# Kernel optimization log

Measured on AMD Instinct MI355X. Metric: run time of the kernel, lower is better.

## Reference

```python
import jax, jax.numpy as jnp
import numpy as np

H2 = 512    # internal hidden = hidden_size*2
E = 128     # embedding_size
V = 50000   # vocabulary_size
L = 512     # max_length (encoder input length)
B = 128     # batch


def setup_inputs() -> dict:
    key = jax.random.key(0)
    ks = jax.random.split(key, 20)
    s = 0.02
    return {
        "input_ids": jax.random.randint(ks[0], (B,), 0, V),
        "hidden": jax.random.normal(ks[1], (1, B, H2), jnp.float32),
        "encoder_outputs": jax.random.normal(ks[2], (L, B, H2), jnp.float32),
        "full_input": jax.random.randint(ks[3], (L, B), 0, V),
        # parameters
        "embedding": jax.random.normal(ks[4], (V, E), jnp.float32) * s,
        "W_ih": jax.random.normal(ks[5], (3 * H2, E), jnp.float32) * s,
        "W_hh": jax.random.normal(ks[6], (3 * H2, H2), jnp.float32) * s,
        "b_ih": jnp.zeros((3 * H2,), jnp.float32),
        "b_hh": jnp.zeros((3 * H2,), jnp.float32),
        "W_ds": jax.random.normal(ks[7], (H2, H2), jnp.float32) * s,
        "b_ds": jnp.zeros((H2,), jnp.float32),
        "w_h": jax.random.normal(ks[8], (H2,), jnp.float32),
        "att_v": jax.random.normal(ks[9], (H2,), jnp.float32),
        "W_oh": jax.random.normal(ks[10], (E, 2 * H2), jnp.float32) * s,
        "b_oh": jnp.zeros((E,), jnp.float32),
        "W_ov": jax.random.normal(ks[11], (V, E), jnp.float32) * s,
        "b_ov": jnp.zeros((V,), jnp.float32),
        "W_ptr": jax.random.normal(ks[12], (1, 2 * H2 + E), jnp.float32) * s,
        "b_ptr": jnp.zeros((1,), jnp.float32),
    }


def reference(input_ids, hidden, encoder_outputs, full_input, embedding,
              W_ih, W_hh, b_ih, b_hh, W_ds, b_ds, w_h, att_v,
              W_oh, b_oh, W_ov, b_ov, W_ptr, b_ptr):
    Bn = input_ids.shape[0]
    Ln = encoder_outputs.shape[0]
    Vn = embedding.shape[0]

    emb = embedding[input_ids]                       # [B, E] (dropout = identity in eval)
    h0 = hidden[0]                                   # [B, 2h]

    # single GRU step (PyTorch gate order r, z, n)
    gx = emb @ W_ih.T + b_ih                         # [B, 3*2h]
    gh = h0 @ W_hh.T + b_hh
    xr, xz, xn = jnp.split(gx, 3, axis=1)
    hr, hz, hn = jnp.split(gh, 3, axis=1)
    r = jax.nn.sigmoid(xr + hr)
    z = jax.nn.sigmoid(xz + hz)
    n = jnp.tanh(xn + r * hn)
    h_new = (1.0 - z) * n + z * h0                   # [B, 2h]

    # Bahdanau-style attention (faithful to source, incl. softmax over dim=1 = batch axis)
    dsl = h_new @ W_ds.T + b_ds                      # [B, 2h]
    att = jnp.tanh(w_h * encoder_outputs + dsl[None])  # [L, B, 2h]
    scores = (att_v * att).sum(-1)                   # [L, B]
    attn = jax.nn.softmax(scores, axis=1)            # torch F.softmax(dim=1)

    context = jnp.einsum('lb,lbh->bh', attn, encoder_outputs)  # [B, 2h]
    combined = jnp.concatenate([h_new, context], axis=1)        # [B, 4h]

    p_vocab = jax.nn.softmax((combined @ W_oh.T + b_oh) @ W_ov.T + b_ov, axis=1)  # [B, V]

    p_gen = jax.nn.sigmoid(jnp.concatenate([combined, emb], axis=1) @ W_ptr.T + b_ptr)  # [B, 1]

    # scatter attention mass onto extended vocab (copy distribution)
    token_input_dist = jnp.zeros((Bn, Vn + Ln), p_vocab.dtype).at[
        jnp.arange(Bn)[:, None], full_input.T
    ].add(attn.T)

    pad = jnp.zeros((Bn, Ln), p_vocab.dtype)
    p_final = jnp.concatenate([p_vocab * p_gen, pad], axis=1) + (1.0 - p_gen) * token_input_dist
    return (p_final, h_new[None], attn)
```

## Files before the change

kernel.cpp:

```cpp
#include <hip/hip_runtime.h>
#include <math.h>

#define B_  128
#define E_  128
#define H2_ 512
#define H3_ 1536
#define L_  512
#define V_  50000
#define VL_ 50512

typedef short bf16x8 __attribute__((ext_vector_type(8)));
typedef float f32x4 __attribute__((ext_vector_type(4)));

__device__ __forceinline__ float fast_tanh(float x) {
    float e = __expf(2.f * x);
    return 1.f - 2.f / (e + 1.f);
}
__device__ __forceinline__ float fast_sigmoid(float x) {
    return 1.f / (1.f + __expf(-x));
}
__device__ __forceinline__ short f2bf(float f) {
    unsigned u = __float_as_uint(f);
    u += 0x7fff + ((u >> 16) & 1);
    return (short)(u >> 16);
}

__global__ void k_gates(const int* __restrict__ ids, const float* __restrict__ tab,
                        const float* __restrict__ hidden,
                        const float* __restrict__ W_ih, const float* __restrict__ W_hh,
                        float* __restrict__ gxp, float* __restrict__ ghp) {
    __shared__ float As[32][36];
    __shared__ float Ws[32][36];
    int z = blockIdx.z;
    int which = (z < 2) ? 0 : 1;
    int kbeg  = which ? (z - 2) * 128 : z * 64;
    int kiter = which ? 4 : 2;
    const float* W = which ? W_hh : W_ih;
    int ldw = which ? H2_ : E_;
    float* C = which ? (ghp + (size_t)(z - 2) * B_ * H3_) : (gxp + (size_t)z * B_ * H3_);
    int bm = blockIdx.x * 32, bn = blockIdx.y * 32;
    int tid = threadIdx.x;
    int tm0 = (tid / 16) * 2, tn0 = (tid % 16) * 2;
    float acc[2][2] = {};
    for (int it = 0; it < kiter; ++it) {
        int k0 = kbeg + it * 32;
        for (int v = tid; v < 256; v += 256) {
            int m = v >> 3, q = (v & 7) << 2;
            int gm = bm + m;
            const float* arow = which ? (hidden + (size_t)gm * H2_)
                                      : (tab + (size_t)ids[gm] * E_);
            float4 x = *(const float4*)(arow + k0 + q);
            As[q+0][m] = x.x; As[q+1][m] = x.y; As[q+2][m] = x.z; As[q+3][m] = x.w;
        }
        for (int v = tid; v < 256; v += 256) {
            int n = v >> 3, q = (v & 7) << 2;
            float4 x = *(const float4*)(W + (size_t)(bn + n) * ldw + k0 + q);
            Ws[q+0][n] = x.x; Ws[q+1][n] = x.y; Ws[q+2][n] = x.z; Ws[q+3][n] = x.w;
        }
        __syncthreads();
        #pragma unroll
        for (int kk = 0; kk < 32; ++kk) {
            float a0 = As[kk][tm0], a1 = As[kk][tm0+1];
            float w0 = Ws[kk][tn0], w1 = Ws[kk][tn0+1];
            acc[0][0] += a0*w0; acc[0][1] += a0*w1;
            acc[1][0] += a1*w0; acc[1][1] += a1*w1;
        }
        __syncthreads();
    }
    #pragma unroll
    for (int i = 0; i < 2; ++i)
        #pragma unroll
        for (int j = 0; j < 2; ++j)
            C[(size_t)(bm+tm0+i) * H3_ + bn+tn0+j] = acc[i][j];
}

template<int BM, int BN, int BK, int TM, int TN, int SPLITK, bool ATOMIC>
__global__ void gemm_t(const float* __restrict__ A, int lda,
                       const float* __restrict__ W, int ldw,
                       float* __restrict__ C, int ldc,
                       int N, int K, int partElems) {
    __shared__ float As[BK][BM + 4];
    __shared__ float Ws[BK][BN + 4];
    int bm = blockIdx.x * BM, bn = blockIdx.y * BN;
    int tid = threadIdx.x;
    constexpr int NT = BN / TN;
    int tm0 = (tid / NT) * TM;
    int tn0 = (tid % NT) * TN;
    int kchunk = K / SPLITK;
    int kbeg = blockIdx.z * kchunk;
    float acc[TM][TN] = {};
    for (int k0 = kbeg; k0 < kbeg + kchunk; k0 += BK) {
        #pragma unroll
        for (int v = tid; v < BM * BK / 4; v += 256) {
            int m = v / (BK / 4), q = (v % (BK / 4)) * 4;
            float4 x = *(const float4*)(A + (size_t)(bm + m) * lda + k0 + q);
            As[q+0][m] = x.x; As[q+1][m] = x.y; As[q+2][m] = x.z; As[q+3][m] = x.w;
        }
        #pragma unroll
        for (int v = tid; v < BN * BK / 4; v += 256) {
            int n = v / (BK / 4), q = (v % (BK / 4)) * 4;
            float4 x = *(const float4*)(W + (size_t)(bn + n) * ldw + k0 + q);
            Ws[q+0][n] = x.x; Ws[q+1][n] = x.y; Ws[q+2][n] = x.z; Ws[q+3][n] = x.w;
        }
        __syncthreads();
        #pragma unroll
        for (int kk = 0; kk < BK; ++kk) {
            float a[TM], w[TN];
            #pragma unroll
            for (int i = 0; i < TM; ++i) a[i] = As[kk][tm0 + i];
            #pragma unroll
            for (int j = 0; j < TN; ++j) w[j] = Ws[kk][tn0 + j];
            #pragma unroll
            for (int i = 0; i < TM; ++i)
                #pragma unroll
                for (int j = 0; j < TN; ++j) acc[i][j] += a[i] * w[j];
        }
        __syncthreads();
    }
    float* Cz = ATOMIC ? C : (C + (size_t)blockIdx.z * partElems);
    #pragma unroll
    for (int i = 0; i < TM; ++i)
        #pragma unroll
        for (int j = 0; j < TN; ++j) {
            if (ATOMIC) atomicAdd(&Cz[(size_t)(bm+tm0+i) * ldc + bn+tn0+j], acc[i][j]);
            else        Cz[(size_t)(bm+tm0+i) * ldc + bn+tn0+j] = acc[i][j];
        }
}

__global__ void k_gru(const float* __restrict__ gxp, const float* __restrict__ ghp,
                      const float* __restrict__ b_ih, const float* __restrict__ b_hh,
                      const float* __restrict__ h0, const float* __restrict__ b_oh,
                      float* __restrict__ comb, float* __restrict__ hout,
                      float* __restrict__ hid, float* __restrict__ rsum8) {
    int idx = blockIdx.x * blockDim.x + threadIdx.x;
    int b = idx >> 9, h = idx & 511;
    const float* gx0 = gxp + (size_t)b * H3_;
    const float* gx1 = gx0 + (size_t)B_ * H3_;
    float xr = gx0[h]         + gx1[h]         + b_ih[h];
    float xz = gx0[H2_+h]     + gx1[H2_+h]     + b_ih[H2_+h];
    float xn = gx0[2*H2_+h]   + gx1[2*H2_+h]   + b_ih[2*H2_+h];
    float hr = b_hh[h], hz = b_hh[H2_+h], hn = b_hh[2*H2_+h];
    #pragma unroll
    for (int z = 0; z < 4; ++z) {
        const float* g = ghp + ((size_t)z * B_ + b) * H3_;
        hr += g[h]; hz += g[H2_+h]; hn += g[2*H2_+h];
    }
    float r = fast_sigmoid(xr + hr);
    float zz = fast_sigmoid(xz + hz);
    float n = fast_tanh(xn + r * hn);
    float hv = (1.f - zz) * n + zz * h0[idx];
    comb[b * (2 * H2_) + h] = hv;
    hout[idx] = hv;
    if (idx < B_ * E_) hid[idx] = b_oh[idx & 127];
    if (idx < 1024)    rsum8[idx] = 0.f;
}

__global__ void k_scores(const float* __restrict__ enc, const float* __restrict__ dslp,
                         const float* __restrict__ b_ds,
                         const float* __restrict__ w_h, const float* __restrict__ att_v,
                         float* __restrict__ scores) {
    int wid = (blockIdx.x << 2) + (threadIdx.x >> 6);
    int lane = threadIdx.x & 63;
    int b = wid & 127, lg = wid >> 7;
    int l0 = lg << 3;
    const float4* w4 = (const float4*)w_h;
    const float4* v4 = (const float4*)att_v;
    const float4* bd4 = (const float4*)b_ds;
    float4 d0 = bd4[lane], d1 = bd4[lane + 64];
    #pragma unroll
    for (int z = 0; z < 4; ++z) {
        const float4* dp = (const float4*)(dslp + (size_t)z * B_ * H2_ + b * H2_);
        float4 p0 = dp[lane], p1 = dp[lane + 64];
        d0.x += p0.x; d0.y += p0.y; d0.z += p0.z; d0.w += p0.w;
        d1.x += p1.x; d1.y += p1.y; d1.z += p1.z; d1.w += p1.w;
    }
    float4 w0 = w4[lane], w1 = w4[lane + 64];
    float4 v0 = v4[lane], v1 = v4[lane + 64];
    float4 e0[8], e1[8];
    #pragma unroll
    for (int q = 0; q < 8; ++q) {
        const float4* e4 = (const float4*)(enc + ((size_t)((l0 + q) * B_ + b)) * H2_);
        e0[q] = e4[lane];
        e1[q] = e4[lane + 64];
    }
    float s[8];
    #pragma unroll
    for (int q = 0; q < 8; ++q) {
        float t;
        t  = v0.x * fast_tanh(w0.x * e0[q].x + d0.x);
        t += v0.y * fast_tanh(w0.y * e0[q].y + d0.y);
        t += v0.z * fast_tanh(w0.z * e0[q].z + d0.z);
        t += v0.w * fast_tanh(w0.w * e0[q].w + d0.w);
        t += v1.x * fast_tanh(w1.x * e1[q].x + d1.x);
        t += v1.y * fast_tanh(w1.y * e1[q].y + d1.y);
        t += v1.z * fast_tanh(w1.z * e1[q].z + d1.z);
        t += v1.w * fast_tanh(w1.w * e1[q].w + d1.w);
        s[q] = t;
    }
    #pragma unroll
    for (int q = 0; q < 8; ++q) {
        float t = s[q];
        #pragma unroll
        for (int o = 32; o; o >>= 1) t += __shfl_xor(t, o);
        if (lane == 0) scores[(l0 + q) * B_ + b] = t;
    }
}

__global__ void k_softmax(const float* __restrict__ scores, float* __restrict__ attn) {
    int l = blockIdx.x, lane = threadIdx.x;
    float s0 = scores[l * B_ + lane], s1 = scores[l * B_ + lane + 64];
    float m = fmaxf(s0, s1);
    #pragma unroll
    for (int o = 32; o; o >>= 1) m = fmaxf(m, __shfl_xor(m, o));
    float e0 = __expf(s0 - m), e1 = __expf(s1 - m);
    float t = e0 + e1;
    #pragma unroll
    for (int o = 32; o; o >>= 1) t += __shfl_xor(t, o);
    float inv = 1.f / t;
    attn[l * B_ + lane] = e0 * inv;
    attn[l * B_ + lane + 64] = e1 * inv;
}

__global__ void k_context(const float* __restrict__ enc, const float* __restrict__ attn,
                          float* __restrict__ ctxp) {
    int b = blockIdx.x;
    int l0 = blockIdx.y << 6;
    int tid = threadIdx.x;
    __shared__ float a_s[64];
    if (tid < 64) a_s[tid] = attn[(l0 + tid) * B_ + b];
    __syncthreads();
    const float4* e = (const float4*)(enc + ((size_t)l0 * B_ + b) * H2_) + tid;
    float4 c = make_float4(0.f, 0.f, 0.f, 0.f);
    #pragma unroll 8
    for (int i = 0; i < 64; ++i) {
        float4 x = e[(size_t)i * (B_ * H2_ / 4)];
        float a = a_s[i];
        c.x += a * x.x; c.y += a * x.y; c.z += a * x.z; c.w += a * x.w;
    }
    ((float4*)(ctxp + ((size_t)blockIdx.y * B_ + b) * H2_))[tid] = c;
}

__global__ void k_ctxpgen(const float* __restrict__ ctxp, const int* __restrict__ ids,
                          const float* __restrict__ tab, const float* __restrict__ W_ptr,
                          const float* __restrict__ b_ptr,
                          float* __restrict__ comb, float* __restrict__ pgen) {
    __shared__ float red[128];
    int b = blockIdx.x, tid = threadIdx.x;
    float4 c = make_float4(0.f, 0.f, 0.f, 0.f);
    #pragma unroll
    for (int z = 0; z < 8; ++z) {
        float4 x = ((const float4*)(ctxp + ((size_t)z * B_ + b) * H2_))[tid];
        c.x += x.x; c.y += x.y; c.z += x.z; c.w += x.w;
    }
    ((float4*)(comb + b * (2 * H2_) + H2_))[tid] = c;
    const float4* wp = (const float4*)W_ptr;
    float4 wc = wp[128 + tid];
    float s = c.x * wc.x + c.y * wc.y + c.z * wc.z + c.w * wc.w;
    float4 hv = ((const float4*)(comb + b * (2 * H2_)))[tid];
    float4 wh = wp[tid];
    s += hv.x * wh.x + hv.y * wh.y + hv.z * wh.z + hv.w * wh.w;
    if (tid < 32) {
        float4 ev = ((const float4*)(tab + (size_t)ids[b] * E_))[tid];
        float4 we = wp[256 + tid];
        s += ev.x * we.x + ev.y * we.y + ev.z * we.z + ev.w * we.w;
    }
    red[tid] = s;
    __syncthreads();
    if (tid < 64) {
        float t = red[tid] + red[tid + 64];
        #pragma unroll
        for (int o = 32; o; o >>= 1) t += __shfl_xor(t, o);
        if (tid == 0) pgen[b] = fast_sigmoid(t + b_ptr[0]);
    }
}

__global__ void k_vsum(const float* __restrict__ hid, const float* __restrict__ Wov,
                       const float* __restrict__ bov, float* __restrict__ rsum8) {
    __shared__ float sm[4][128];
    int L = threadIdx.x & 63, w = threadIdx.x >> 6;
    int lrow = L & 15, lk = L >> 4;
    int n0 = blockIdx.x * 128 + w * 32;

    bf16x8 bfr[2][4];
    #pragma unroll
    for (int nt = 0; nt < 2; ++nt) {
        int n = n0 + nt * 16 + lrow;
        #pragma unroll
        for (int kk = 0; kk < 4; ++kk) {
            bf16x8 f;
            if (n < V_) {
                const float* p = Wov + (size_t)n * 128 + kk * 32 + lk * 8;
                float4 x = *(const float4*)p, y = *(const float4*)(p + 4);
                f[0]=f2bf(x.x); f[1]=f2bf(x.y); f[2]=f2bf(x.z); f[3]=f2bf(x.w);
                f[4]=f2bf(y.x); f[5]=f2bf(y.y); f[6]=f2bf(y.z); f[7]=f2bf(y.w);
            } else {
                #pragma unroll
                for (int j = 0; j < 8; ++j) f[j] = 0;
            }
            bfr[nt][kk] = f;
        }
    }
    f32x4 acc[8][2] = {};
    #pragma unroll
    for (int mt = 0; mt < 8; ++mt) {
        bf16x8 afr[4];
        #pragma unroll
        for (int kk = 0; kk < 4; ++kk) {
            const float* p = hid + (size_t)(mt * 16 + lrow) * 128 + kk * 32 + lk * 8;
            float4 x = *(const float4*)p, y = *(const float4*)(p + 4);
            bf16x8 f;
            f[0]=f2bf(x.x); f[1]=f2bf(x.y); f[2]=f2bf(x.z); f[3]=f2bf(x.w);
            f[4]=f2bf(y.x); f[5]=f2bf(y.y); f[6]=f2bf(y.z); f[7]=f2bf(y.w);
            afr[kk] = f;
        }
        #pragma unroll
        for (int nt = 0; nt < 2; ++nt)
            #pragma unroll
            for (int kk = 0; kk < 4; ++kk)
                acc[mt][nt] = __builtin_amdgcn_mfma_f32_16x16x32_bf16(
                    afr[kk], bfr[nt][kk], acc[mt][nt], 0, 0, 0);
    }
    float bv[2];
    #pragma unroll
    for (int nt = 0; nt < 2; ++nt) {
        int n = n0 + nt * 16 + lrow;
        bv[nt] = (n < V_) ? bov[n] : 0.f;
    }
    float rs[8][4];
    #pragma unroll
    for (int mt = 0; mt < 8; ++mt) {
        #pragma unroll
        for (int r = 0; r < 4; ++r) rs[mt][r] = 0.f;
        #pragma unroll
        for (int nt = 0; nt < 2; ++nt) {
            int n = n0 + nt * 16 + lrow;
            if (n < V_) {
                #pragma unroll
                for (int r = 0; r < 4; ++r)
                    rs[mt][r] += __expf(acc[mt][nt][r] + bv[nt]);
            }
        }
    }
    #pragma unroll
    for (int o = 1; o < 16; o <<= 1)
        #pragma unroll
        for (int mt = 0; mt < 8; ++mt)
            #pragma unroll
            for (int r = 0; r < 4; ++r) rs[mt][r] += __shfl_xor(rs[mt][r], o);
    if (lrow == 0) {
        #pragma unroll
        for (int mt = 0; mt < 8; ++mt)
            #pragma unroll
            for (int r = 0; r < 4; ++r)
                sm[w][mt * 16 + lk * 4 + r] = rs[mt][r];
    }
    __syncthreads();
    if (threadIdx.x < 128) {
        float p = sm[0][threadIdx.x] + sm[1][threadIdx.x]
                + sm[2][threadIdx.x] + sm[3][threadIdx.x];
        atomicAdd(&rsum8[(blockIdx.x & 7) * 128 + threadIdx.x], p);
    }
}

__global__ void k_vwrite(const float* __restrict__ hid, const float* __restrict__ Wov,
                         const float* __restrict__ bov, const float* __restrict__ pgen,
                         const float* __restrict__ rsum8, float* __restrict__ out) {
    __shared__ float scs[128];
    if (blockIdx.x == 391) {
        for (int i = threadIdx.x; i < B_ * (L_ / 4); i += 256) {
            int b = i >> 7, k = i & 127;
            ((float4*)(out + (size_t)b * VL_ + V_))[k] = make_float4(0.f,0.f,0.f,0.f);
        }
        return;
    }
    if (threadIdx.x < 128) {
        float s = 0.f;
        #pragma unroll
        for (int j = 0; j < 8; ++j) s += rsum8[j * 128 + threadIdx.x];
        scs[threadIdx.x] = pgen[threadIdx.x] / s;
    }
    __syncthreads();
    int L = threadIdx.x & 63, w = threadIdx.x >> 6;
    int lrow = L & 15, lk = L >> 4;
    int n0 = blockIdx.x * 128 + w * 32;

    bf16x8 bfr[2][4];
    #pragma unroll
    for (int nt = 0; nt < 2; ++nt) {
        int n = n0 + nt * 16 + lrow;
        #pragma unroll
        for (int kk = 0; kk < 4; ++kk) {
            bf16x8 f;
            if (n < V_) {
                const float* p = Wov + (size_t)n * 128 + kk * 32 + lk * 8;
                float4 x = *(const float4*)p, y = *(const float4*)(p + 4);
                f[0]=f2bf(x.x); f[1]=f2bf(x.y); f[2]=f2bf(x.z); f[3]=f2bf(x.w);
                f[4]=f2bf(y.x); f[5]=f2bf(y.y); f[6]=f2bf(y.z); f[7]=f2bf(y.w);
            } else {
                #pragma unroll
                for (int j = 0; j < 8; ++j) f[j] = 0;
            }
            bfr[nt][kk] = f;
        }
    }
    f32x4 acc[8][2] = {};
    #pragma unroll
    for (int mt = 0; mt < 8; ++mt) {
        bf16x8 afr[4];
        #pragma unroll
        for (int kk = 0; kk < 4; ++kk) {
            const float* p = hid + (size_t)(mt * 16 + lrow) * 128 + kk * 32 + lk * 8;
            float4 x = *(const float4*)p, y = *(const float4*)(p + 4);
            bf16x8 f;
            f[0]=f2bf(x.x); f[1]=f2bf(x.y); f[2]=f2bf(x.z); f[3]=f2bf(x.w);
            f[4]=f2bf(y.x); f[5]=f2bf(y.y); f[6]=f2bf(y.z); f[7]=f2bf(y.w);
            afr[kk] = f;
        }
        #pragma unroll
        for (int nt = 0; nt < 2; ++nt)
            #pragma unroll
            for (int kk = 0; kk < 4; ++kk)
                acc[mt][nt] = __builtin_amdgcn_mfma_f32_16x16x32_bf16(
                    afr[kk], bfr[nt][kk], acc[mt][nt], 0, 0, 0);
    }
    float bv[2];
    #pragma unroll
    for (int nt = 0; nt < 2; ++nt) {
        int n = n0 + nt * 16 + lrow;
        bv[nt] = (n < V_) ? bov[n] : 0.f;
    }
    #pragma unroll
    for (int mt = 0; mt < 8; ++mt) {
        #pragma unroll
        for (int nt = 0; nt < 2; ++nt) {
            int n = n0 + nt * 16 + lrow;
            if (n < V_) {
                #pragma unroll
                for (int r = 0; r < 4; ++r) {
                    int row = mt * 16 + lk * 4 + r;
                    out[(size_t)row * VL_ + n] =
                        __expf(acc[mt][nt][r] + bv[nt]) * scs[row];
                }
            }
        }
    }
}

__global__ void k_scatter(float* __restrict__ out, const int* __restrict__ full_input,
                          const float* __restrict__ attn, const float* __restrict__ pgen) {
    int idx = blockIdx.x * blockDim.x + threadIdx.x;
    int b = idx & 127;
    int tok = full_input[idx];
    atomicAdd(&out[(size_t)b * VL_ + tok], (1.f - pgen[b]) * attn[idx]);
}

extern "C" void kernel_launch(void* const* d_in, const int* in_sizes, int n_in,
                              void* d_out, int out_size, void* d_ws, size_t ws_size,
                              hipStream_t stream) {
    const int*   input_ids = (const int*)d_in[0];
    const float* hidden    = (const float*)d_in[1];
    const float* enc       = (const float*)d_in[2];
    const int*   full_in   = (const int*)d_in[3];
    const float* emb_tab   = (const float*)d_in[4];
    const float* W_ih      = (const float*)d_in[5];
    const float* W_hh      = (const float*)d_in[6];
    const float* b_ih      = (const float*)d_in[7];
    const float* b_hh      = (const float*)d_in[8];
    const float* W_ds      = (const float*)d_in[9];
    const float* b_ds      = (const float*)d_in[10];
    const float* w_h       = (const float*)d_in[11];
    const float* att_v     = (const float*)d_in[12];
    const float* W_oh      = (const float*)d_in[13];
    const float* b_oh      = (const float*)d_in[14];
    const float* W_ov      = (const float*)d_in[15];
    const float* b_ov      = (const float*)d_in[16];
    const float* W_ptr     = (const float*)d_in[17];
    const float* b_ptr     = (const float*)d_in[18];

    float* out = (float*)d_out;
    float* p_final = out;
    float* h_out   = out + (size_t)B_ * VL_;
    float* attn    = out + (size_t)B_ * VL_ + B_ * H2_;

    float* ws = (float*)d_ws;
    float* gxp    = ws;
    float* ghp    = gxp + 393216;
    float* comb   = ghp + 786432;
    float* dslp   = comb + 131072;
    float* scores = dslp + 262144;
    float* ctxp   = scores + 65536;
    float* hid    = ctxp + 524288;
    float* pgen   = hid + 16384;
    float* rsum8  = pgen + 128;

    k_gates<<<dim3(4,48,6), dim3(256), 0, stream>>>(input_ids, emb_tab, hidden,
                                                    W_ih, W_hh, gxp, ghp);
    k_gru<<<dim3(256), dim3(256), 0, stream>>>(gxp, ghp, b_ih, b_hh, hidden, b_oh,
                                               comb, h_out, hid, rsum8);
    gemm_t<32,32,32,2,2,4,false><<<dim3(4,16,4), dim3(256), 0, stream>>>(
        comb, 2*H2_, W_ds, H2_, dslp, H2_, H2_, H2_, B_*H2_);
    k_scores<<<dim3(2048), dim3(256), 0, stream>>>(enc, dslp, b_ds, w_h, att_v, scores);
    k_softmax<<<dim3(L_), dim3(64), 0, stream>>>(scores, attn);
    k_context<<<dim3(B_, 8), dim3(128), 0, stream>>>(enc, attn, ctxp);
    k_ctxpgen<<<dim3(B_), dim3(128), 0, stream>>>(ctxp, input_ids, emb_tab,
                                                  W_ptr, b_ptr, comb, pgen);
    gemm_t<32,32,32,2,2,8,true><<<dim3(4,4,8), dim3(256), 0, stream>>>(
        comb, 2*H2_, W_oh, 2*H2_, hid, E_, E_, 2*H2_, 0);
    k_vsum<<<dim3(391), dim3(256), 0, stream>>>(hid, W_ov, b_ov, rsum8);
    k_vwrite<<<dim3(392), dim3(256), 0, stream>>>(hid, W_ov, b_ov, pgen, rsum8, p_final);
    k_scatter<<<dim3(L_*B_/256), dim3(256), 0, stream>>>(p_final, full_in, attn, pgen);
}
```

Before: 140.6 us.

## Fuse attention scores, softmax and context into one kernel; fold W_oh into pgen

Merges the score, softmax and context kernels into a single k_attn kernel. Each block handles 4 encoder positions across the whole batch, so the batch-axis softmax can be done in shared memory and the encoder tile is re-read while still in cache. The W_ds GEMM now accumulates atomically into a bias-initialised buffer instead of writing split-K partials, and the W_oh projection moves into the context/pgen kernel. This removes several launches and the intermediate score and partial buffers. In exchange, the context reduction now sums 128 partials per batch row instead of 8, and the W_oh matvec runs serially per thread.

```diff
diff --git a/kernel.cpp b/kernel.cpp
--- a/kernel.cpp
+++ b/kernel.cpp
@@ -74,11 +74,10 @@
             C[(size_t)(bm+tm0+i) * H3_ + bn+tn0+j] = acc[i][j];
 }
 
-template<int BM, int BN, int BK, int TM, int TN, int SPLITK, bool ATOMIC>
-__global__ void gemm_t(const float* __restrict__ A, int lda,
-                       const float* __restrict__ W, int ldw,
-                       float* __restrict__ C, int ldc,
-                       int N, int K, int partElems) {
+template<int BM, int BN, int BK, int TM, int TN, int SPLITK>
+__global__ void gemm_atomic(const float* __restrict__ A, int lda,
+                            const float* __restrict__ W, int ldw,
+                            float* __restrict__ C, int ldc, int N, int K) {
     __shared__ float As[BK][BM + 4];
     __shared__ float Ws[BK][BN + 4];
     int bm = blockIdx.x * BM, bn = blockIdx.y * BN;
@@ -117,21 +116,18 @@
         }
         __syncthreads();
     }
-    float* Cz = ATOMIC ? C : (C + (size_t)blockIdx.z * partElems);
     #pragma unroll
     for (int i = 0; i < TM; ++i)
         #pragma unroll
-        for (int j = 0; j < TN; ++j) {
-            if (ATOMIC) atomicAdd(&Cz[(size_t)(bm+tm0+i) * ldc + bn+tn0+j], acc[i][j]);
-            else        Cz[(size_t)(bm+tm0+i) * ldc + bn+tn0+j] = acc[i][j];
-        }
+        for (int j = 0; j < TN; ++j)
+            atomicAdd(&C[(size_t)(bm+tm0+i) * ldc + bn+tn0+j], acc[i][j]);
 }
 
 __global__ void k_gru(const float* __restrict__ gxp, const float* __restrict__ ghp,
                       const float* __restrict__ b_ih, const float* __restrict__ b_hh,
-                      const float* __restrict__ h0, const float* __restrict__ b_oh,
+                      const float* __restrict__ h0, const float* __restrict__ b_ds,
                       float* __restrict__ comb, float* __restrict__ hout,
-                      float* __restrict__ hid, float* __restrict__ rsum8) {
+                      float* __restrict__ dsl, float* __restrict__ rsum8) {
     int idx = blockIdx.x * blockDim.x + threadIdx.x;
     int b = idx >> 9, h = idx & 511;
     const float* gx0 = gxp + (size_t)b * H3_;
@@ -151,127 +147,122 @@
     float hv = (1.f - zz) * n + zz * h0[idx];
     comb[b * (2 * H2_) + h] = hv;
     hout[idx] = hv;
-    if (idx < B_ * E_) hid[idx] = b_oh[idx & 127];
-    if (idx < 1024)    rsum8[idx] = 0.f;
-}
-
-__global__ void k_scores(const float* __restrict__ enc, const float* __restrict__ dslp,
-                         const float* __restrict__ b_ds,
-                         const float* __restrict__ w_h, const float* __restrict__ att_v,
-                         float* __restrict__ scores) {
-    int wid = (blockIdx.x << 2) + (threadIdx.x >> 6);
-    int lane = threadIdx.x & 63;
-    int b = wid & 127, lg = wid >> 7;
-    int l0 = lg << 3;
-    const float4* w4 = (const float4*)w_h;
-    const float4* v4 = (const float4*)att_v;
-    const float4* bd4 = (const float4*)b_ds;
-    float4 d0 = bd4[lane], d1 = bd4[lane + 64];
-    #pragma unroll
-    for (int z = 0; z < 4; ++z) {
-        const float4* dp = (const float4*)(dslp + (size_t)z * B_ * H2_ + b * H2_);
-        float4 p0 = dp[lane], p1 = dp[lane + 64];
-        d0.x += p0.x; d0.y += p0.y; d0.z += p0.z; d0.w += p0.w;
-        d1.x += p1.x; d1.y += p1.y; d1.z += p1.z; d1.w += p1.w;
-    }
-    float4 w0 = w4[lane], w1 = w4[lane + 64];
-    float4 v0 = v4[lane], v1 = v4[lane + 64];
-    float4 e0[8], e1[8];
-    #pragma unroll
-    for (int q = 0; q < 8; ++q) {
-        const float4* e4 = (const float4*)(enc + ((size_t)((l0 + q) * B_ + b)) * H2_);
-        e0[q] = e4[lane];
-        e1[q] = e4[lane + 64];
-    }
-    float s[8];
-    #pragma unroll
-    for (int q = 0; q < 8; ++q) {
-        float t;
-        t  = v0.x * fast_tanh(w0.x * e0[q].x + d0.x);
-        t += v0.y * fast_tanh(w0.y * e0[q].y + d0.y);
-        t += v0.z * fast_tanh(w0.z * e0[q].z + d0.z);
-        t += v0.w * fast_tanh(w0.w * e0[q].w + d0.w);
-        t += v1.x * fast_tanh(w1.x * e1[q].x + d1.x);
-        t += v1.y * fast_tanh(w1.y * e1[q].y + d1.y);
-        t += v1.z * fast_tanh(w1.z * e1[q].z + d1.z);
-        t += v1.w * fast_tanh(w1.w * e1[q].w + d1.w);
-        s[q] = t;
-    }
-    #pragma unroll
-    for (int q = 0; q < 8; ++q) {
-        float t = s[q];
-        #pragma unroll
-        for (int o = 32; o; o >>= 1) t += __shfl_xor(t, o);
-        if (lane == 0) scores[(l0 + q) * B_ + b] = t;
-    }
-}
-
-__global__ void k_softmax(const float* __restrict__ scores, float* __restrict__ attn) {
-    int l = blockIdx.x, lane = threadIdx.x;
-    float s0 = scores[l * B_ + lane], s1 = scores[l * B_ + lane + 64];
-    float m = fmaxf(s0, s1);
-    #pragma unroll
-    for (int o = 32; o; o >>= 1) m = fmaxf(m, __shfl_xor(m, o));
-    float e0 = __expf(s0 - m), e1 = __expf(s1 - m);
-    float t = e0 + e1;
-    #pragma unroll
-    for (int o = 32; o; o >>= 1) t += __shfl_xor(t, o);
-    float inv = 1.f / t;
-    attn[l * B_ + lane] = e0 * inv;
-    attn[l * B_ + lane + 64] = e1 * inv;
-}
-
-__global__ void k_context(const float* __restrict__ enc, const float* __restrict__ attn,
-                          float* __restrict__ ctxp) {
-    int b = blockIdx.x;
-    int l0 = blockIdx.y << 6;
-    int tid = threadIdx.x;
-    __shared__ float a_s[64];
-    if (tid < 64) a_s[tid] = attn[(l0 + tid) * B_ + b];
-    __syncthreads();
-    const float4* e = (const float4*)(enc + ((size_t)l0 * B_ + b) * H2_) + tid;
-    float4 c = make_float4(0.f, 0.f, 0.f, 0.f);
-    #pragma unroll 8
-    for (int i = 0; i < 64; ++i) {
-        float4 x = e[(size_t)i * (B_ * H2_ / 4)];
-        float a = a_s[i];
-        c.x += a * x.x; c.y += a * x.y; c.z += a * x.z; c.w += a * x.w;
-    }
-    ((float4*)(ctxp + ((size_t)blockIdx.y * B_ + b) * H2_))[tid] = c;
-}
-
-__global__ void k_ctxpgen(const float* __restrict__ ctxp, const int* __restrict__ ids,
-                          const float* __restrict__ tab, const float* __restrict__ W_ptr,
-                          const float* __restrict__ b_ptr,
-                          float* __restrict__ comb, float* __restrict__ pgen) {
+    dsl[idx] = b_ds[h];
+    if (idx < 1024) rsum8[idx] = 0.f;
+}
+
+__global__ __launch_bounds__(1024, 4)
+void k_attn(const float* __restrict__ enc, const float* __restrict__ dsl,
+            const float* __restrict__ w_h, const float* __restrict__ att_v,
+            float* __restrict__ attn, float* __restrict__ pctx) {
+    __shared__ float sp[8][16][2];
+    __shared__ float attn_lds[128];
+    int t = threadIdx.x;
+    int g = t >> 7;
+    int h4 = t & 127;
+    int lane = t & 63;
+    int w2 = (t >> 6) & 1;
+    float4 wv = ((const float4*)w_h)[h4];
+    float4 vv = ((const float4*)att_v)[h4];
+    float4 acc[16];
+    #pragma unroll
+    for (int i = 0; i < 16; ++i) acc[i] = make_float4(0.f, 0.f, 0.f, 0.f);
+    int l0 = blockIdx.x << 2;
+    for (int lj = 0; lj < 4; ++lj) {
+        int l = l0 + lj;
+        #pragma unroll
+        for (int i = 0; i < 16; ++i) {
+            int b = g + (i << 3);
+            float4 e = ((const float4*)enc)[((size_t)l * B_ + b) * 128 + h4];
+            float4 d = ((const float4*)dsl)[b * 128 + h4];
+            float p;
+            p  = vv.x * fast_tanh(wv.x * e.x + d.x);
+            p += vv.y * fast_tanh(wv.y * e.y + d.y);
+            p += vv.z * fast_tanh(wv.z * e.z + d.z);
+            p += vv.w * fast_tanh(wv.w * e.w + d.w);
+            #pragma unroll
+            for (int o = 32; o; o >>= 1) p += __shfl_xor(p, o);
+            if (lane == 0) sp[g][i][w2] = p;
+        }
+        __syncthreads();
+        if (t < 64) {
+            int b1 = t + 64;
+            float s0 = sp[t & 7][t >> 3][0] + sp[t & 7][t >> 3][1];
+            float s1 = sp[t & 7][(t >> 3) + 8][0] + sp[t & 7][(t >> 3) + 8][1];
+            float m = fmaxf(s0, s1);
+            #pragma unroll
+            for (int o = 32; o; o >>= 1) m = fmaxf(m, __shfl_xor(m, o));
+            float e0 = __expf(s0 - m), e1 = __expf(s1 - m);
+            float tt = e0 + e1;
+            #pragma unroll
+            for (int o = 32; o; o >>= 1) tt += __shfl_xor(tt, o);
+            float inv = 1.f / tt;
+            attn_lds[t]  = e0 * inv;
+            attn_lds[b1] = e1 * inv;
+            attn[l * B_ + t]  = e0 * inv;
+            attn[l * B_ + b1] = e1 * inv;
+        }
+        __syncthreads();
+        #pragma unroll
+        for (int i = 0; i < 16; ++i) {
+            int b = g + (i << 3);
+            float4 e = ((const float4*)enc)[((size_t)l * B_ + b) * 128 + h4];
+            float a = attn_lds[b];
+            acc[i].x += a * e.x; acc[i].y += a * e.y;
+            acc[i].z += a * e.z; acc[i].w += a * e.w;
+        }
+    }
+    #pragma unroll
+    for (int i = 0; i < 16; ++i) {
+        int b = g + (i << 3);
+        ((float4*)pctx)[(size_t)blockIdx.x * 16384 + b * 128 + h4] = acc[i];
+    }
+}
+
+__global__ void k_cph(const float* __restrict__ pctx, const int* __restrict__ ids,
+                      const float* __restrict__ tab, const float* __restrict__ W_ptr,
+                      const float* __restrict__ b_ptr, const float* __restrict__ W_oh,
+                      const float* __restrict__ b_oh,
+                      float* __restrict__ comb, float* __restrict__ pgen,
+                      float* __restrict__ hid) {
+    __shared__ float cmb[1024];
     __shared__ float red[128];
     int b = blockIdx.x, tid = threadIdx.x;
     float4 c = make_float4(0.f, 0.f, 0.f, 0.f);
-    #pragma unroll
-    for (int z = 0; z < 8; ++z) {
-        float4 x = ((const float4*)(ctxp + ((size_t)z * B_ + b) * H2_))[tid];
+    #pragma unroll 8
+    for (int z = 0; z < 128; ++z) {
+        float4 x = ((const float4*)pctx)[(size_t)z * 16384 + b * 128 + tid];
         c.x += x.x; c.y += x.y; c.z += x.z; c.w += x.w;
     }
     ((float4*)(comb + b * (2 * H2_) + H2_))[tid] = c;
+    ((float4*)(cmb + H2_))[tid] = c;
+    float4 hn = ((const float4*)(comb + b * (2 * H2_)))[tid];
+    ((float4*)cmb)[tid] = hn;
     const float4* wp = (const float4*)W_ptr;
-    float4 wc = wp[128 + tid];
-    float s = c.x * wc.x + c.y * wc.y + c.z * wc.z + c.w * wc.w;
-    float4 hv = ((const float4*)(comb + b * (2 * H2_)))[tid];
-    float4 wh = wp[tid];
-    s += hv.x * wh.x + hv.y * wh.y + hv.z * wh.z + hv.w * wh.w;
+    float4 wh = wp[tid], wc = wp[128 + tid];
+    float s = hn.x*wh.x + hn.y*wh.y + hn.z*wh.z + hn.w*wh.w
+            + c.x*wc.x + c.y*wc.y + c.z*wc.z + c.w*wc.w;
     if (tid < 32) {
         float4 ev = ((const float4*)(tab + (size_t)ids[b] * E_))[tid];
         float4 we = wp[256 + tid];
-        s += ev.x * we.x + ev.y * we.y + ev.z * we.z + ev.w * we.w;
+        s += ev.x*we.x + ev.y*we.y + ev.z*we.z + ev.w*we.w;
     }
     red[tid] = s;
     __syncthreads();
     if (tid < 64) {
-        float t = red[tid] + red[tid + 64];
-        #pragma unroll
-        for (int o = 32; o; o >>= 1) t += __shfl_xor(t, o);
-        if (tid == 0) pgen[b] = fast_sigmoid(t + b_ptr[0]);
-    }
+        float tt = red[tid] + red[tid + 64];
+        #pragma unroll
+        for (int o = 32; o; o >>= 1) tt += __shfl_xor(tt, o);
+        if (tid == 0) pgen[b] = fast_sigmoid(tt + b_ptr[0]);
+    }
+    float acc = b_oh[tid];
+    const float4* wr = (const float4*)(W_oh + (size_t)tid * (2 * H2_));
+    #pragma unroll 8
+    for (int k = 0; k < 256; ++k) {
+        float4 ww = wr[k];
+        acc += cmb[k*4+0]*ww.x + cmb[k*4+1]*ww.y + cmb[k*4+2]*ww.z + cmb[k*4+3]*ww.w;
+    }
+    hid[b * E_ + tid] = acc;
 }
 
 __global__ void k_vsum(const float* __restrict__ hid, const float* __restrict__ Wov,
@@ -280,7 +271,6 @@
     int L = threadIdx.x & 63, w = threadIdx.x >> 6;
     int lrow = L & 15, lk = L >> 4;
     int n0 = blockIdx.x * 128 + w * 32;
-
     bf16x8 bfr[2][4];
     #pragma unroll
     for (int nt = 0; nt < 2; ++nt) {
@@ -383,7 +373,6 @@
     int L = threadIdx.x & 63, w = threadIdx.x >> 6;
     int lrow = L & 15, lk = L >> 4;
     int n0 = blockIdx.x * 128 + w * 32;
-
     bf16x8 bfr[2][4];
     #pragma unroll
     for (int nt = 0; nt < 2; ++nt) {
@@ -486,26 +475,21 @@
     float* gxp    = ws;
     float* ghp    = gxp + 393216;
     float* comb   = ghp + 786432;
-    float* dslp   = comb + 131072;
-    float* scores = dslp + 262144;
-    float* ctxp   = scores + 65536;
-    float* hid    = ctxp + 524288;
+    float* dsl    = comb + 131072;
+    float* hid    = dsl + 65536;
     float* pgen   = hid + 16384;
     float* rsum8  = pgen + 128;
+    float* pctx   = rsum8 + 1024;
 
     k_gates<<<dim3(4,48,6), dim3(256), 0, stream>>>(input_ids, emb_tab, hidden,
                                                     W_ih, W_hh, gxp, ghp);
-    k_gru<<<dim3(256), dim3(256), 0, stream>>>(gxp, ghp, b_ih, b_hh, hidden, b_oh,
-                                               comb, h_out, hid, rsum8);
-    gemm_t<32,32,32,2,2,4,false><<<dim3(4,16,4), dim3(256), 0, stream>>>(
-        comb, 2*H2_, W_ds, H2_, dslp, H2_, H2_, H2_, B_*H2_);
-    k_scores<<<dim3(2048), dim3(256), 0, stream>>>(enc, dslp, b_ds, w_h, att_v, scores);
-    k_softmax<<<dim3(L_), dim3(64), 0, stream>>>(scores, attn);
-    k_context<<<dim3(B_, 8), dim3(128), 0, stream>>>(enc, attn, ctxp);
-    k_ctxpgen<<<dim3(B_), dim3(128), 0, stream>>>(ctxp, input_ids, emb_tab,
-                                                  W_ptr, b_ptr, comb, pgen);
-    gemm_t<32,32,32,2,2,8,true><<<dim3(4,4,8), dim3(256), 0, stream>>>(
-        comb, 2*H2_, W_oh, 2*H2_, hid, E_, E_, 2*H2_, 0);
+    k_gru<<<dim3(256), dim3(256), 0, stream>>>(gxp, ghp, b_ih, b_hh, hidden, b_ds,
+                                               comb, h_out, dsl, rsum8);
+    gemm_atomic<32,32,32,2,2,4><<<dim3(4,16,4), dim3(256), 0, stream>>>(
+        comb, 2*H2_, W_ds, H2_, dsl, H2_, H2_, H2_);
+    k_attn<<<dim3(L_/4), dim3(1024), 0, stream>>>(enc, dsl, w_h, att_v, attn, pctx);
+    k_cph<<<dim3(B_), dim3(128), 0, stream>>>(pctx, input_ids, emb_tab, W_ptr, b_ptr,
+                                              W_oh, b_oh, comb, pgen, hid);
     k_vsum<<<dim3(391), dim3(256), 0, stream>>>(hid, W_ov, b_ov, rsum8);
     k_vwrite<<<dim3(392), dim3(256), 0, stream>>>(hid, W_ov, b_ov, pgen, rsum8, p_final);
     k_scatter<<<dim3(L_*B_/256), dim3(256), 0, stream>>>(p_final, full_in, attn, pgen);
```

New measurement: 233.9 us. 1.66x slower.

## Fuse attention softmax into context kernel and split vocab-sum over batch halves

Applied to the files above, without the earlier changes.

Removes the standalone softmax kernel. Each context block loads its 64-row slice of scores into shared memory, normalises it over the batch axis, and uses the result directly. Block b==0 also writes attn out for the later scatter. This duplicates softmax work across 128 blocks and uses 32KB of shared memory per block in exchange for one fewer launch and no attn round-trip. Separately, the vocab-sum kernel is split over two batch halves, doubling the grid and halving per-block accumulators to raise occupancy, at the cost of loading and converting W_ov twice.

```diff
diff --git a/kernel.cpp b/kernel.cpp
--- a/kernel.cpp
+++ b/kernel.cpp
@@ -206,38 +206,47 @@
     }
 }
 
-__global__ void k_softmax(const float* __restrict__ scores, float* __restrict__ attn) {
-    int l = blockIdx.x, lane = threadIdx.x;
-    float s0 = scores[l * B_ + lane], s1 = scores[l * B_ + lane + 64];
-    float m = fmaxf(s0, s1);
-    #pragma unroll
-    for (int o = 32; o; o >>= 1) m = fmaxf(m, __shfl_xor(m, o));
-    float e0 = __expf(s0 - m), e1 = __expf(s1 - m);
-    float t = e0 + e1;
-    #pragma unroll
-    for (int o = 32; o; o >>= 1) t += __shfl_xor(t, o);
-    float inv = 1.f / t;
-    attn[l * B_ + lane] = e0 * inv;
-    attn[l * B_ + lane + 64] = e1 * inv;
-}
-
-__global__ void k_context(const float* __restrict__ enc, const float* __restrict__ attn,
-                          float* __restrict__ ctxp) {
-    int b = blockIdx.x;
-    int l0 = blockIdx.y << 6;
-    int tid = threadIdx.x;
-    __shared__ float a_s[64];
-    if (tid < 64) a_s[tid] = attn[(l0 + tid) * B_ + b];
+__global__ void k_sctx(const float* __restrict__ enc, const float* __restrict__ scores,
+                       float* __restrict__ attn, float* __restrict__ ctxp) {
+    __shared__ float sa[64 * 128];
+    int b = blockIdx.x, ly = blockIdx.y;
+    int t = threadIdx.x;
+    int l0 = ly << 6;
+    float4* sa4 = (float4*)sa;
+    const float4* sc4 = (const float4*)(scores + l0 * B_);
+    #pragma unroll
+    for (int i = t; i < 64 * 32; i += 128) sa4[i] = sc4[i];
     __syncthreads();
-    const float4* e = (const float4*)(enc + ((size_t)l0 * B_ + b) * H2_) + tid;
+    {
+        int l = t >> 1, half = t & 1;
+        float* row = sa + l * 128 + half * 64;
+        float m = -1e30f;
+        #pragma unroll 8
+        for (int j = 0; j < 64; ++j) m = fmaxf(m, row[j]);
+        m = fmaxf(m, __shfl_xor(m, 1));
+        float s = 0.f;
+        #pragma unroll 8
+        for (int j = 0; j < 64; ++j) s += __expf(row[j] - m);
+        s += __shfl_xor(s, 1);
+        float inv = 1.f / s;
+        #pragma unroll 8
+        for (int j = 0; j < 64; ++j) row[j] = __expf(row[j] - m) * inv;
+    }
+    __syncthreads();
+    if (b == 0) {
+        float4* a4 = (float4*)(attn + l0 * B_);
+        #pragma unroll
+        for (int i = t; i < 64 * 32; i += 128) a4[i] = sa4[i];
+    }
+    const float4* e = (const float4*)(enc + ((size_t)l0 * B_ + b) * H2_) + t;
     float4 c = make_float4(0.f, 0.f, 0.f, 0.f);
     #pragma unroll 8
     for (int i = 0; i < 64; ++i) {
         float4 x = e[(size_t)i * (B_ * H2_ / 4)];
-        float a = a_s[i];
+        float a = sa[i * 128 + b];
         c.x += a * x.x; c.y += a * x.y; c.z += a * x.z; c.w += a * x.w;
     }
-    ((float4*)(ctxp + ((size_t)blockIdx.y * B_ + b) * H2_))[tid] = c;
+    ((float4*)(ctxp + ((size_t)ly * B_ + b) * H2_))[t] = c;
 }
 
 __global__ void k_ctxpgen(const float* __restrict__ ctxp, const int* __restrict__ ids,
@@ -276,11 +285,11 @@
 
 __global__ void k_vsum(const float* __restrict__ hid, const float* __restrict__ Wov,
                        const float* __restrict__ bov, float* __restrict__ rsum8) {
-    __shared__ float sm[4][128];
+    __shared__ float sm[4][64];
     int L = threadIdx.x & 63, w = threadIdx.x >> 6;
     int lrow = L & 15, lk = L >> 4;
     int n0 = blockIdx.x * 128 + w * 32;
-
+    int mb = blockIdx.y * 64;
     bf16x8 bfr[2][4];
     #pragma unroll
     for (int nt = 0; nt < 2; ++nt) {
@@ -300,13 +309,13 @@
             bfr[nt][kk] = f;
         }
     }
-    f32x4 acc[8][2] = {};
-    #pragma unroll
-    for (int mt = 0; mt < 8; ++mt) {
+    f32x4 acc[4][2] = {};
+    #pragma unroll
+    for (int mt = 0; mt < 4; ++mt) {
         bf16x8 afr[4];
         #pragma unroll
         for (int kk = 0; kk < 4; ++kk) {
-            const float* p = hid + (size_t)(mt * 16 + lrow) * 128 + kk * 32 + lk * 8;
+            const float* p = hid + (size_t)(mb + mt * 16 + lrow) * 128 + kk * 32 + lk * 8;
             float4 x = *(const float4*)p, y = *(const float4*)(p + 4);
             bf16x8 f;
             f[0]=f2bf(x.x); f[1]=f2bf(x.y); f[2]=f2bf(x.z); f[3]=f2bf(x.w);
@@ -326,9 +335,9 @@
         int n = n0 + nt * 16 + lrow;
         bv[nt] = (n < V_) ? bov[n] : 0.f;
     }
-    float rs[8][4];
-    #pragma unroll
-    for (int mt = 0; mt < 8; ++mt) {
+    float rs[4][4];
+    #pragma unroll
+    for (int mt = 0; mt < 4; ++mt) {
         #pragma unroll
         for (int r = 0; r < 4; ++r) rs[mt][r] = 0.f;
         #pragma unroll
@@ -344,21 +353,21 @@
     #pragma unroll
     for (int o = 1; o < 16; o <<= 1)
         #pragma unroll
-        for (int mt = 0; mt < 8; ++mt)
+        for (int mt = 0; mt < 4; ++mt)
             #pragma unroll
             for (int r = 0; r < 4; ++r) rs[mt][r] += __shfl_xor(rs[mt][r], o);
     if (lrow == 0) {
         #pragma unroll
-        for (int mt = 0; mt < 8; ++mt)
+        for (int mt = 0; mt < 4; ++mt)
             #pragma unroll
             for (int r = 0; r < 4; ++r)
                 sm[w][mt * 16 + lk * 4 + r] = rs[mt][r];
     }
     __syncthreads();
-    if (threadIdx.x < 128) {
+    if (threadIdx.x < 64) {
         float p = sm[0][threadIdx.x] + sm[1][threadIdx.x]
                 + sm[2][threadIdx.x] + sm[3][threadIdx.x];
-        atomicAdd(&rsum8[(blockIdx.x & 7) * 128 + threadIdx.x], p);
+        atomicAdd(&rsum8[(blockIdx.x & 7) * 128 + mb + threadIdx.x], p);
     }
 }
 
@@ -383,7 +392,6 @@
     int L = threadIdx.x & 63, w = threadIdx.x >> 6;
     int lrow = L & 15, lk = L >> 4;
     int n0 = blockIdx.x * 128 + w * 32;
-
     bf16x8 bfr[2][4];
     #pragma unroll
     for (int nt = 0; nt < 2; ++nt) {
@@ -500,13 +508,12 @@
     gemm_t<32,32,32,2,2,4,false><<<dim3(4,16,4), dim3(256), 0, stream>>>(
         comb, 2*H2_, W_ds, H2_, dslp, H2_, H2_, H2_, B_*H2_);
     k_scores<<<dim3(2048), dim3(256), 0, stream>>>(enc, dslp, b_ds, w_h, att_v, scores);
-    k_softmax<<<dim3(L_), dim3(64), 0, stream>>>(scores, attn);
-    k_context<<<dim3(B_, 8), dim3(128), 0, stream>>>(enc, attn, ctxp);
+    k_sctx<<<dim3(B_, 8), dim3(128), 0, stream>>>(enc, scores, attn, ctxp);
     k_ctxpgen<<<dim3(B_), dim3(128), 0, stream>>>(ctxp, input_ids, emb_tab,
                                                   W_ptr, b_ptr, comb, pgen);
     gemm_t<32,32,32,2,2,8,true><<<dim3(4,4,8), dim3(256), 0, stream>>>(
         comb, 2*H2_, W_oh, 2*H2_, hid, E_, E_, 2*H2_, 0);
-    k_vsum<<<dim3(391), dim3(256), 0, stream>>>(hid, W_ov, b_ov, rsum8);
+    k_vsum<<<dim3(391, 2), dim3(256), 0, stream>>>(hid, W_ov, b_ov, rsum8);
     k_vwrite<<<dim3(392), dim3(256), 0, stream>>>(hid, W_ov, b_ov, pgen, rsum8, p_final);
     k_scatter<<<dim3(L_*B_/256), dim3(256), 0, stream>>>(p_final, full_in, attn, pgen);
 }
```

Result: slower. 159.4 us (+13.4%).
